# Kernel optimization log

Measured on AMD Instinct MI355X. Metric: run time of the kernel, lower is better.

The kernel has to match this reference:

```python
import jax, jax.numpy as jnp
import numpy as np

N, E, E3, DIM = 25000, 50000, 40000, 64


def setup_inputs() -> dict:
    key = jax.random.key(0)
    ks = jax.random.split(key, 16)
    def g(k, shape, scale=0.1):
        return jax.random.normal(k, shape, jnp.float32) * scale
    return {
        "x": jax.random.normal(ks[0], (N, 8), jnp.float32),
        "edge_attr": jax.random.uniform(ks[1], (E, 19), dtype=jnp.float32),
        "edge_attr3": jax.random.uniform(ks[2], (E3, 8), dtype=jnp.float32),
        "edge_index": jax.random.randint(ks[3], (2, E), 0, N),
        "edge_index3": jax.random.randint(ks[4], (2, E3), 0, N),
        "W_node": g(ks[5], (8, DIM)), "b_node": jnp.zeros((DIM,), jnp.float32),
        "W_ea": g(ks[6], (19, 12)), "b_ea": jnp.zeros((12,), jnp.float32),
        "W_e1": g(ks[7], (12, 128)), "b_e1": jnp.zeros((128,), jnp.float32),
        "W_e2": g(ks[8], (128, DIM * DIM), 0.01), "b_e2": jnp.zeros((DIM * DIM,), jnp.float32),
        "conv_bias": jnp.zeros((DIM,), jnp.float32),
        "W_ih": g(ks[9], (3 * DIM, DIM)), "b_ih": jnp.zeros((3 * DIM,), jnp.float32),
        "W_hh": g(ks[10], (3 * DIM, DIM)), "b_hh": jnp.zeros((3 * DIM,), jnp.float32),
        "W_l1": g(ks[11], (DIM + 8, 128)), "b_l1": jnp.zeros((128,), jnp.float32),
        "W_l2": g(ks[12], (128, 1)), "b_l2": jnp.zeros((1,), jnp.float32),
    }


def _forward(x, edge_attr, edge_attr3,
             W_node, b_node, W_ea, b_ea, W_e1, b_e1, W_e2, b_e2, conv_bias,
             W_ih, b_ih, W_hh, b_hh, W_l1, b_l1, W_l2, b_l2,
             edge_index, edge_index3):
    dim = W_node.shape[1]
    n = x.shape[0]
    out = jax.nn.relu(x @ W_node + b_node)                      # [N, dim]
    ea = jax.nn.relu(edge_attr @ W_ea + b_ea)                   # [E, 12]
    # edge MLP -> per-edge dim x dim weight matrices (same for all 3 conv calls)
    Wedge = (jax.nn.relu(ea @ W_e1 + b_e1) @ W_e2 + b_e2).reshape(-1, dim, dim)  # [E, dim, dim]
    src, dst = edge_index[0], edge_index[1]
    ones = jnp.ones((src.shape[0],), x.dtype)
    cnt = jnp.maximum(jax.ops.segment_sum(ones, dst, num_segments=n), 1.0)  # [N]
    h = out
    for _ in range(3):
        msg = jnp.einsum('ed,edf->ef', out[src], Wedge)                     # per-edge GEMV
        agg = jax.ops.segment_sum(msg, dst, num_segments=n) / cnt[:, None]  # scatter-mean
        m = jax.nn.relu(agg + conv_bias)
        # single-step GRU (PyTorch gate order: r, z, n)
        gi = m @ W_ih.T + b_ih
        gh = h @ W_hh.T + b_hh
        ir, iz, inn = jnp.split(gi, 3, axis=-1)
        hr, hz, hn = jnp.split(gh, 3, axis=-1)
        r = jax.nn.sigmoid(ir + hr)
        z = jax.nn.sigmoid(iz + hz)
        ng = jnp.tanh(inn + r * hn)
        h = (1.0 - z) * ng + z * h
        out = h
    pair = (out[edge_index3[0]] + out[edge_index3[1]]) * 0.5    # mean over the 2 endpoints
    yhat = jnp.concatenate([pair, edge_attr3], axis=1)          # [E3, dim+8]
    yhat = jax.nn.relu(yhat @ W_l1 + b_l1) @ W_l2 + b_l2        # [E3, 1]
    return yhat[:, 0]


def reference(x, edge_attr, edge_attr3, edge_index, edge_index3,
              W_node, b_node, W_ea, b_ea, W_e1, b_e1, W_e2, b_e2, conv_bias,
              W_ih, b_ih, W_hh, b_hh, W_l1, b_l1, W_l2, b_l2):
    return _forward(x, edge_attr, edge_attr3,
                    W_node, b_node, W_ea, b_ea, W_e1, b_e1, W_e2, b_e2, conv_bias,
                    W_ih, b_ih, W_hh, b_hh, W_l1, b_l1, W_l2, b_l2,
                    edge_index, edge_index3)
```

## Files before the change

kernel.cpp:

```cpp
#include <hip/hip_runtime.h>

typedef unsigned short u16;
typedef unsigned int u32;
typedef __attribute__((ext_vector_type(8))) short short8v;
typedef __attribute__((ext_vector_type(4))) float float4v;

__device__ __forceinline__ float sigm(float x) { return 1.0f / (1.0f + __expf(-x)); }
__device__ __forceinline__ u16 f2bf(float f) {
  u32 u = __float_as_uint(f);
  u32 r = (u + 0x7fffu + ((u >> 16) & 1u)) >> 16;
  return (u16)r;
}
__device__ __forceinline__ float bf2f(u16 w) { return __uint_as_float(((u32)w) << 16); }

__global__ void k_cnt(const int* __restrict__ dst, int* __restrict__ cnt, int E) {
  int e = blockIdx.x * blockDim.x + threadIdx.x;
  if (e < E) atomicAdd(&cnt[dst[e]], 1);
}

__global__ void k_scan1(const int* __restrict__ cnt, int* __restrict__ bsum, int N) {
  __shared__ int ws[4];
  int t = threadIdx.x;
  int i = blockIdx.x * 256 + t;
  int v = (i < N) ? cnt[i] : 0;
  int s = v;
  for (int off = 1; off < 64; off <<= 1) s += __shfl_xor(s, off);
  int wid = t >> 6, lane = t & 63;
  if (lane == 0) ws[wid] = s;
  __syncthreads();
  if (t == 0) bsum[blockIdx.x] = ws[0] + ws[1] + ws[2] + ws[3];
}

__global__ void k_scan2(int* __restrict__ bsum, int* __restrict__ row, int nb, int N) {
  __shared__ int s[256];
  int t = threadIdx.x;
  if (t < nb) s[t] = bsum[t];
  __syncthreads();
  if (t == 0) {
    int run = 0;
    for (int i = 0; i < nb; ++i) { int x = s[i]; s[i] = run; run += x; }
    row[N] = run;
  }
  __syncthreads();
  if (t < nb) bsum[t] = s[t];
}

__global__ void k_scan3(const int* __restrict__ cnt, const int* __restrict__ bsum,
                        int* __restrict__ row, int* __restrict__ cursor, int N) {
  __shared__ int ws[4];
  int t = threadIdx.x;
  int i = blockIdx.x * 256 + t;
  int v = (i < N) ? cnt[i] : 0;
  int lane = t & 63, wid = t >> 6;
  int incl = v;
  for (int off = 1; off < 64; off <<= 1) {
    int u = __shfl_up(incl, off);
    if (lane >= off) incl += u;
  }
  if (lane == 63) ws[wid] = incl;
  __syncthreads();
  int woff = bsum[blockIdx.x];
  for (int w = 0; w < wid; ++w) woff += ws[w];
  int excl = woff + incl - v;
  if (i < N) { row[i] = excl; cursor[i] = excl; }
}

__global__ void k_pos(const int* __restrict__ dst, int* __restrict__ cursor,
                      int* __restrict__ pos, int E) {
  int e = blockIdx.x * blockDim.x + threadIdx.x;
  if (e < E) pos[e] = atomicAdd(&cursor[dst[e]], 1);
}

__global__ __launch_bounds__(256) void k_edge_mlp(
    const float* __restrict__ ea_in, const float* __restrict__ Wea,
    const float* __restrict__ bea, const float* __restrict__ We1,
    const float* __restrict__ be1, u16* __restrict__ Ahi, int E) {
  __shared__ float att[2][19];
  __shared__ float ea[2][12];
  int half = threadIdx.x >> 7;
  int t = threadIdx.x & 127;
  int e = blockIdx.x * 2 + half;
  bool real = (e < E);
  int ee = real ? e : E - 1;
  if (t < 19) att[half][t] = ea_in[(size_t)ee * 19 + t];
  __syncthreads();
  if (t < 12) {
    float a = bea[t];
#pragma unroll
    for (int k = 0; k < 19; ++k) a += att[half][k] * Wea[k * 12 + t];
    ea[half][t] = fmaxf(a, 0.0f);
  }
  __syncthreads();
  float a = be1[t];
#pragma unroll
  for (int j = 0; j < 12; ++j) a += ea[half][j] * We1[j * 128 + t];
  if (real) Ahi[(size_t)e * 128 + t] = f2bf(fmaxf(a, 0.0f));
}

__global__ void k_prep_all(
    const float* __restrict__ x, const float* __restrict__ Wn,
    const float* __restrict__ bn, float* __restrict__ h, int N, int nbNode,
    const float* __restrict__ W2, u16* __restrict__ Bph, int nbPack,
    const float* __restrict__ Wih, const float* __restrict__ Whh,
    u16* __restrict__ WpI, u16* __restrict__ WpH, int nbWtf,
    const float* __restrict__ Wl1, u16* __restrict__ Wp1) {
  int b = blockIdx.x;
  if (b < nbNode) {
    int tid = b * 256 + threadIdx.x;
    if (tid >= N * 64) return;
    int n = tid >> 6, f = tid & 63;
    float acc = bn[f];
    for (int k = 0; k < 8; ++k) acc += x[(size_t)n * 8 + k] * Wn[k * 64 + f];
    h[tid] = fmaxf(acc, 0.0f);
  } else if (b < nbNode + nbPack) {
    int tid = (b - nbNode) * 256 + threadIdx.x;
    if (tid >= 128 * 4096) return;
    int j = tid & 7;
    int lane = (tid >> 3) & 63;
    int nt = (tid >> 9) & 3;
    int ks = (tid >> 11) & 3;
    int d = tid >> 13;
    int c = lane & 15, q = lane >> 4;
    int k = ks * 32 + q * 8 + j;
    int n = d * 64 + nt * 16 + c;
    Bph[tid] = f2bf(W2[(size_t)k * 4096 + n]);
  } else if (b < nbNode + nbPack + nbWtf) {
    int tid = (b - nbNode - nbPack) * 256 + threadIdx.x;
    if (tid >= 2 * 12288) return;
    int w = tid / 12288;
    int r = tid - w * 12288;
    int jj = r & 7;
    int lane = (r >> 3) & 63;
    int t = r >> 9;
    int nt = t % 12, ks = t / 12;
    int c = lane & 15, q = lane >> 4;
    int j = nt * 16 + c;
    int k = ks * 32 + q * 8 + jj;
    const float* W = w ? Whh : Wih;
    u16* Wp = w ? WpH : WpI;
    Wp[r] = f2bf(W[j * 64 + k]);
  } else {
    int tid = (b - nbNode - nbPack - nbWtf) * 256 + threadIdx.x;
    if (tid >= 3 * 8 * 64 * 8) return;
    int j = tid & 7;
    int lane = (tid >> 3) & 63;
    int nt = (tid >> 9) & 7;
    int ks = tid >> 12;
    int c = lane & 15, q = lane >> 4;
    int k = ks * 32 + q * 8 + j;
    int n = nt * 16 + c;
    Wp1[tid] = f2bf((k < 72) ? Wl1[k * 128 + n] : 0.0f);
  }
}

__global__ __launch_bounds__(256, 3) void k_conv_fused(
    const u16* __restrict__ Ahi, const u16* __restrict__ Bph,
    const float* __restrict__ b2, const float* __restrict__ h,
    const int* __restrict__ src, const int* __restrict__ pos,
    float* __restrict__ msgp, int E) {
  __shared__ __align__(16) u16 sB[2][8192];
  __shared__ __align__(16) float hsT[32 * 132];
  int m0 = blockIdx.x * 128;
  int d0 = blockIdx.y * 32;
  int tid = threadIdx.x;
  int wave = tid >> 6, lane = tid & 63;
  int mw = wave >> 1, fw = wave & 1;
  int c = lane & 15, q = lane >> 4;

  auto stageB = [&](int d, int b) {
    const u16* gp = Bph + (size_t)d * 8192 + wave * 2048 + lane * 8;
    u16* lp = &sB[b][wave * 2048];
#pragma unroll
    for (int i = 0; i < 4; ++i)
      __builtin_amdgcn_global_load_lds(
          (const __attribute__((address_space(1))) unsigned int*)(gp + i * 512),
          (__attribute__((address_space(3))) unsigned int*)(lp + i * 512), 16, 0, 0);
  };

  stageB(d0, 0);

  short8v afr[4][4];
#pragma unroll
  for (int mt = 0; mt < 4; ++mt) {
    int gr = m0 + mw * 64 + mt * 16 + c;
    if (gr >= E) gr = E - 1;
    const u16* ap = Ahi + (size_t)gr * 128 + q * 8;
#pragma unroll
    for (int ks = 0; ks < 4; ++ks) afr[mt][ks] = *(const short8v*)(ap + ks * 32);
  }

#pragma unroll
  for (int p = 0; p < 4; ++p) {
    int slot = p * 256 + tid;
    int r = slot >> 3, s = slot & 7;
    int ge = m0 + r;
    if (ge >= E) ge = E - 1;
    int sn = src[ge];
    float4 v = *(const float4*)(h + (size_t)sn * 64 + d0 + s * 4);
    hsT[(s * 4 + 0) * 132 + r] = v.x;
    hsT[(s * 4 + 1) * 132 + r] = v.y;
    hsT[(s * 4 + 2) * 132 + r] = v.z;
    hsT[(s * 4 + 3) * 132 + r] = v.w;
  }
  float b2v0 = b2[(size_t)d0 * 64 + fw * 32 + c];
  float b2v1 = b2[(size_t)d0 * 64 + fw * 32 + 16 + c];
  __syncthreads();

  float msg[4][2][4];
#pragma unroll
  for (int mt = 0; mt < 4; ++mt)
#pragma unroll
    for (int nt = 0; nt < 2; ++nt)
#pragma unroll
      for (int r = 0; r < 4; ++r) msg[mt][nt][r] = 0.0f;

  int cur = 0;
  for (int dl = 0; dl < 32; ++dl) {
    float nb0 = 0.f, nb1 = 0.f;
    if (dl < 31) {
      stageB(d0 + dl + 1, cur ^ 1);
      nb0 = b2[(size_t)(d0 + dl + 1) * 64 + fw * 32 + c];
      nb1 = b2[(size_t)(d0 + dl + 1) * 64 + fw * 32 + 16 + c];
    }
    float4v acc[4][2];
#pragma unroll
    for (int mt = 0; mt < 4; ++mt)
#pragma unroll
      for (int nt = 0; nt < 2; ++nt) acc[mt][nt] = (float4v){0.f, 0.f, 0.f, 0.f};
    __builtin_amdgcn_s_setprio(1);
#pragma unroll
    for (int ks = 0; ks < 4; ++ks) {
      short8v b0 = *(const short8v*)(&sB[cur][ks * 2048 + fw * 1024 + lane * 8]);
      short8v b1 = *(const short8v*)(&sB[cur][ks * 2048 + fw * 1024 + 512 + lane * 8]);
#pragma unroll
      for (int mt = 0; mt < 4; ++mt) {
        acc[mt][0] = __builtin_amdgcn_mfma_f32_16x16x32_bf16(afr[mt][ks], b0, acc[mt][0], 0, 0, 0);
        acc[mt][1] = __builtin_amdgcn_mfma_f32_16x16x32_bf16(afr[mt][ks], b1, acc[mt][1], 0, 0, 0);
      }
    }
    __builtin_amdgcn_s_setprio(0);
#pragma unroll
    for (int mt = 0; mt < 4; ++mt) {
      float4 hd4 = *(const float4*)(&hsT[dl * 132 + mw * 64 + mt * 16 + q * 4]);
      float hd[4] = {hd4.x, hd4.y, hd4.z, hd4.w};
#pragma unroll
      for (int r = 0; r < 4; ++r) {
        msg[mt][0][r] += hd[r] * (acc[mt][0][r] + b2v0);
        msg[mt][1][r] += hd[r] * (acc[mt][1][r] + b2v1);
      }
    }
    __syncthreads();
    b2v0 = nb0; b2v1 = nb1;
    cur ^= 1;
  }

#pragma unroll
  for (int mt = 0; mt < 4; ++mt) {
#pragma unroll
    for (int r = 0; r < 4; ++r) {
      int e = m0 + mw * 64 + mt * 16 + q * 4 + r;
      if (e < E) {
        int pe = pos[e];
        float* mp = msgp + (size_t)pe * 128 + blockIdx.y * 64 + fw * 32 + c;
#pragma unroll
        for (int nt = 0; nt < 2; ++nt) mp[nt * 16] = msg[mt][nt][r];
      }
    }
  }
}

__global__ __launch_bounds__(256, 2) void k_gru_mfma(
    const float* __restrict__ msgp, const int* __restrict__ row,
    const float* __restrict__ cb, const u16* __restrict__ WpI,
    const u16* __restrict__ WpH, const float* __restrict__ bih,
    const float* __restrict__ bhh, const float* __restrict__ hin,
    float* __restrict__ hout, int N) {
  __shared__ __align__(16) u16 sM[64 * 72];
  __shared__ __align__(16) u16 sH[64 * 72];
  __shared__ __align__(16) float sHf[64 * 68];
  __shared__ int sRow[65];
  int n0 = blockIdx.x * 64;
  int tid = threadIdx.x;
  if (tid < 65) {
    int idx = n0 + tid;
    sRow[tid] = row[(idx <= N) ? idx : N];
  }
  __syncthreads();
  {
    int nl = tid >> 4, fq = tid & 15;
    float4 cbv = *(const float4*)(cb + fq * 4);
#pragma unroll
    for (int pass = 0; pass < 4; ++pass) {
      int n = pass * 16 + nl;
      int gn = n0 + n;
      bool real = (gn < N);
      int b0 = sRow[n], b1 = sRow[n + 1];
      if (!real) b1 = b0;
      float4 av = {0.f, 0.f, 0.f, 0.f};
      for (int j = b0; j < b1; ++j) {
        float4 m0 = *(const float4*)(msgp + (size_t)j * 128 + fq * 4);
        float4 m1 = *(const float4*)(msgp + (size_t)j * 128 + 64 + fq * 4);
        av.x += m0.x + m1.x; av.y += m0.y + m1.y;
        av.z += m0.z + m1.z; av.w += m0.w + m1.w;
      }
      float cf = fmaxf((float)(b1 - b0), 1.0f);
      int hgn = real ? gn : N - 1;
      float4 hv = *(const float4*)(hin + (size_t)hgn * 64 + fq * 4);
      float m0v = fmaxf(av.x / cf + cbv.x, 0.0f);
      float m1v = fmaxf(av.y / cf + cbv.y, 0.0f);
      float m2v = fmaxf(av.z / cf + cbv.z, 0.0f);
      float m3v = fmaxf(av.w / cf + cbv.w, 0.0f);
      ushort4 mu; mu.x = f2bf(m0v); mu.y = f2bf(m1v); mu.z = f2bf(m2v); mu.w = f2bf(m3v);
      ushort4 hu; hu.x = f2bf(hv.x); hu.y = f2bf(hv.y); hu.z = f2bf(hv.z); hu.w = f2bf(hv.w);
      *(ushort4*)(&sM[n * 72 + fq * 4]) = mu;
      *(ushort4*)(&sH[n * 72 + fq * 4]) = hu;
      *(float4*)(&sHf[n * 68 + fq * 4]) = hv;
    }
  }
  __syncthreads();
  int wave = tid >> 6, lane = tid & 63;
  int c = lane & 15, q = lane >> 4;
  short8v am[2], ah[2];
#pragma unroll
  for (int ks = 0; ks < 2; ++ks) {
    am[ks] = *(const short8v*)(&sM[(wave * 16 + c) * 72 + ks * 32 + q * 8]);
    ah[ks] = *(const short8v*)(&sH[(wave * 16 + c) * 72 + ks * 32 + q * 8]);
  }
  float4v accRZ[8], accN[4], accHN[4];
#pragma unroll
  for (int i = 0; i < 8; ++i) accRZ[i] = (float4v){0.f, 0.f, 0.f, 0.f};
#pragma unroll
  for (int i = 0; i < 4; ++i) {
    accN[i] = (float4v){0.f, 0.f, 0.f, 0.f};
    accHN[i] = (float4v){0.f, 0.f, 0.f, 0.f};
  }
#pragma unroll
  for (int ks = 0; ks < 2; ++ks) {
#pragma unroll
    for (int nt = 0; nt < 8; ++nt) {
      short8v bI = *(const short8v*)(WpI + ((size_t)(ks * 12 + nt) * 64 + lane) * 8);
      short8v bH = *(const short8v*)(WpH + ((size_t)(ks * 12 + nt) * 64 + lane) * 8);
      accRZ[nt] = __builtin_amdgcn_mfma_f32_16x16x32_bf16(am[ks], bI, accRZ[nt], 0, 0, 0);
      accRZ[nt] = __builtin_amdgcn_mfma_f32_16x16x32_bf16(ah[ks], bH, accRZ[nt], 0, 0, 0);
    }
#pragma unroll
    for (int nt = 0; nt < 4; ++nt) {
      short8v bI = *(const short8v*)(WpI + ((size_t)(ks * 12 + 8 + nt) * 64 + lane) * 8);
      short8v bH = *(const short8v*)(WpH + ((size_t)(ks * 12 + 8 + nt) * 64 + lane) * 8);
      accN[nt] = __builtin_amdgcn_mfma_f32_16x16x32_bf16(am[ks], bI, accN[nt], 0, 0, 0);
      accHN[nt] = __builtin_amdgcn_mfma_f32_16x16x32_bf16(ah[ks], bH, accHN[nt], 0, 0, 0);
    }
  }
#pragma unroll
  for (int nt = 0; nt < 4; ++nt) {
    int f = nt * 16 + c;
    float brz_r = bih[f] + bhh[f];
    float brz_z = bih[64 + f] + bhh[64 + f];
    float bin = bih[128 + f];
    float bhn = bhh[128 + f];
#pragma unroll
    for (int r = 0; r < 4; ++r) {
      int nl = wave * 16 + q * 4 + r;
      int gn = n0 + nl;
      float rr = sigm(accRZ[nt][r] + brz_r);
      float zz = sigm(accRZ[nt + 4][r] + brz_z);
      float ng = tanhf(accN[nt][r] + bin + rr * (accHN[nt][r] + bhn));
      float hv = sHf[nl * 68 + f];
      if (gn < N) hout[(size_t)gn * 64 + f] = (1.0f - zz) * ng + zz * hv;
    }
  }
}

__global__ __launch_bounds__(256) void k_final_mfma(
    const float* __restrict__ h, const float* __restrict__ ea3,
    const int* __restrict__ idx3, const u16* __restrict__ Wp1,
    const float* __restrict__ bl1, const float* __restrict__ Wl2,
    const float* __restrict__ bl2, float* __restrict__ out, int E3) {
  __shared__ __align__(16) u16 sF[64 * 104];
  int e0 = blockIdx.x * 64;
  int tid = threadIdx.x;
  {
    int er = tid >> 2;
    int part = tid & 3;
    int ge = e0 + er;
    int gc = (ge < E3) ? ge : E3 - 1;
    int a = idx3[gc], b = idx3[E3 + gc];
    const float* pa = h + (size_t)a * 64 + part * 16;
    const float* pb = h + (size_t)b * 64 + part * 16;
#pragma unroll
    for (int u = 0; u < 4; ++u) {
      float4 va = *(const float4*)(pa + u * 4);
      float4 vb = *(const float4*)(pb + u * 4);
      ushort4 mu;
      mu.x = f2bf(0.5f * (va.x + vb.x));
      mu.y = f2bf(0.5f * (va.y + vb.y));
      mu.z = f2bf(0.5f * (va.z + vb.z));
      mu.w = f2bf(0.5f * (va.w + vb.w));
      *(ushort4*)(&sF[er * 104 + part * 16 + u * 4]) = mu;
    }
    if (part == 0) {
      float4 e0v = *(const float4*)(ea3 + (size_t)gc * 8);
      float4 e1v = *(const float4*)(ea3 + (size_t)gc * 8 + 4);
      ushort4 u0, u1;
      u0.x = f2bf(e0v.x); u0.y = f2bf(e0v.y); u0.z = f2bf(e0v.z); u0.w = f2bf(e0v.w);
      u1.x = f2bf(e1v.x); u1.y = f2bf(e1v.y); u1.z = f2bf(e1v.z); u1.w = f2bf(e1v.w);
      *(ushort4*)(&sF[er * 104 + 64]) = u0;
      *(ushort4*)(&sF[er * 104 + 68]) = u1;
    } else {
      ushort4 z = {0, 0, 0, 0};
      *(ushort4*)(&sF[er * 104 + 72 + (part - 1) * 8]) = z;
      *(ushort4*)(&sF[er * 104 + 76 + (part - 1) * 8]) = z;
    }
  }
  __syncthreads();
  int wave = tid >> 6, lane = tid & 63;
  int c = lane & 15, q = lane >> 4;
  float4v acc[8];
#pragma unroll
  for (int nt = 0; nt < 8; ++nt) acc[nt] = (float4v){0.f, 0.f, 0.f, 0.f};
#pragma unroll
  for (int ks = 0; ks < 3; ++ks) {
    short8v af = *(const short8v*)(&sF[(wave * 16 + c) * 104 + ks * 32 + q * 8]);
#pragma unroll
    for (int nt = 0; nt < 8; ++nt) {
      short8v bf = *(const short8v*)(Wp1 + ((size_t)(ks * 8 + nt) * 64 + lane) * 8);
      acc[nt] = __builtin_amdgcn_mfma_f32_16x16x32_bf16(af, bf, acc[nt], 0, 0, 0);
    }
  }
  float v[4] = {0.f, 0.f, 0.f, 0.f};
#pragma unroll
  for (int nt = 0; nt < 8; ++nt) {
    int n = nt * 16 + c;
    float b1 = bl1[n];
    float w2 = Wl2[n];
#pragma unroll
    for (int r = 0; r < 4; ++r) v[r] += fmaxf(acc[nt][r] + b1, 0.0f) * w2;
  }
#pragma unroll
  for (int off = 1; off < 16; off <<= 1) {
#pragma unroll
    for (int r = 0; r < 4; ++r) v[r] += __shfl_xor(v[r], off);
  }
  if (c == 0) {
    float b2v = bl2[0];
#pragma unroll
    for (int r = 0; r < 4; ++r) {
      int e = e0 + wave * 16 + q * 4 + r;
      if (e < E3) out[e] = v[r] + b2v;
    }
  }
}

extern "C" void kernel_launch(void* const* d_in, const int* in_sizes, int n_in,
                              void* d_out, int out_size, void* d_ws, size_t ws_size,
                              hipStream_t stream) {
  const float* x          = (const float*)d_in[0];
  const float* edge_attr  = (const float*)d_in[1];
  const float* edge_attr3 = (const float*)d_in[2];
  const int*   edge_index = (const int*)d_in[3];
  const int*   edge_index3= (const int*)d_in[4];
  const float* W_node = (const float*)d_in[5];
  const float* b_node = (const float*)d_in[6];
  const float* W_ea   = (const float*)d_in[7];
  const float* b_ea   = (const float*)d_in[8];
  const float* W_e1   = (const float*)d_in[9];
  const float* b_e1   = (const float*)d_in[10];
  const float* W_e2   = (const float*)d_in[11];
  const float* b_e2   = (const float*)d_in[12];
  const float* conv_bias = (const float*)d_in[13];
  const float* W_ih   = (const float*)d_in[14];
  const float* b_ih   = (const float*)d_in[15];
  const float* W_hh   = (const float*)d_in[16];
  const float* b_hh   = (const float*)d_in[17];
  const float* W_l1   = (const float*)d_in[18];
  const float* b_l1   = (const float*)d_in[19];
  const float* W_l2   = (const float*)d_in[20];
  const float* b_l2   = (const float*)d_in[21];

  int N  = in_sizes[0] / 8;
  int E  = in_sizes[1] / 19;
  int E3 = in_sizes[2] / 8;

  char* p = (char*)d_ws;
  auto carve = [&](size_t bytes) -> void* {
    char* q = p;
    p += (bytes + 255) & ~(size_t)255;
    return (void*)q;
  };
  float* hA    = (float*)carve((size_t)N * 64 * 4);
  float* hB    = (float*)carve((size_t)N * 64 * 4);
  float* msgp  = (float*)carve((size_t)E * 128 * 4);
  int*   cnt   = (int*)carve((size_t)N * 4);
  int*   row   = (int*)carve((size_t)(N + 1) * 4);
  int*   cursor= (int*)carve((size_t)N * 4);
  int*   pos   = (int*)carve((size_t)E * 4);
  int*   bsum  = (int*)carve(256 * 4);
  u16*   Ahi   = (u16*)carve((size_t)E * 128 * 2);
  u16*   Bph   = (u16*)carve((size_t)128 * 4096 * 2);
  u16*   WpI   = (u16*)carve(12288 * 2);
  u16*   WpH   = (u16*)carve(12288 * 2);
  u16*   Wp1   = (u16*)carve(12288 * 2);

  const int* src = edge_index;
  const int* dst = edge_index + E;

  int nb = (N + 255) / 256;
  hipMemsetAsync(cnt, 0, (size_t)N * 4, stream);
  k_cnt<<<(E + 255) / 256, 256, 0, stream>>>(dst, cnt, E);
  k_scan1<<<nb, 256, 0, stream>>>(cnt, bsum, N);
  k_scan2<<<1, 256, 0, stream>>>(bsum, row, nb, N);
  k_scan3<<<nb, 256, 0, stream>>>(cnt, bsum, row, cursor, N);
  k_pos<<<(E + 255) / 256, 256, 0, stream>>>(dst, cursor, pos, E);

  k_edge_mlp<<<(E + 1) / 2, 256, 0, stream>>>(edge_attr, W_ea, b_ea, W_e1, b_e1, Ahi, E);
  int nbNode = ((size_t)N * 64 + 255) / 256;
  int nbPack = (128 * 4096 + 255) / 256;
  int nbWtf  = (2 * 12288 + 255) / 256;
  int nbWl1  = (12288 + 255) / 256;
  k_prep_all<<<nbNode + nbPack + nbWtf + nbWl1, 256, 0, stream>>>(
      x, W_node, b_node, hA, N, nbNode, W_e2, Bph, nbPack,
      W_ih, W_hh, WpI, WpH, nbWtf, W_l1, Wp1);

  float* hcur = hA;
  float* hnxt = hB;
  dim3 gconv((E + 127) / 128, 2);
  int ngru = (N + 63) / 64;
  for (int it = 0; it < 3; ++it) {
    k_conv_fused<<<gconv, 256, 0, stream>>>(Ahi, Bph, b_e2, hcur, src, pos, msgp, E);
    k_gru_mfma<<<ngru, 256, 0, stream>>>(msgp, row, conv_bias, WpI, WpH,
                                         b_ih, b_hh, hcur, hnxt, N);
    float* tmp = hcur; hcur = hnxt; hnxt = tmp;
  }
  k_final_mfma<<<(E3 + 63) / 64, 256, 0, stream>>>(hcur, edge_attr3, edge_index3, Wp1,
                                                   b_l1, W_l2, b_l2, (float*)d_out, E3);
}
```

Before: 444.6 us.

## Merge conv d-split into one block, store bf16 messages, stage bias in LDS

The conv kernel no longer splits the 64 input dims across two blocks in y. Each block now loops over all 64 dims, so the two fp32 partial message halves are no longer written and summed later. Messages are stored once per edge as bf16, which cuts the write and the GRU gather traffic by about four times. The b_e2 bias is converted to bf16 and kept in LDS instead of being read per iteration. In exchange there is half the grid parallelism, more LDS, lower occupancy (launch bounds 2), and bf16 rounding on the messages and bias.

```diff
diff --git a/kernel.cpp b/kernel.cpp
--- a/kernel.cpp
+++ b/kernel.cpp
@@ -153,15 +153,15 @@
   }
 }
 
-__global__ __launch_bounds__(256, 3) void k_conv_fused(
+__global__ __launch_bounds__(256, 2) void k_conv_fused(
     const u16* __restrict__ Ahi, const u16* __restrict__ Bph,
     const float* __restrict__ b2, const float* __restrict__ h,
     const int* __restrict__ src, const int* __restrict__ pos,
-    float* __restrict__ msgp, int E) {
+    u16* __restrict__ msgh, int E) {
   __shared__ __align__(16) u16 sB[2][8192];
-  __shared__ __align__(16) float hsT[32 * 132];
+  __shared__ __align__(16) float hsT[64 * 132];
+  __shared__ __align__(16) u16 sb2h[4096];
   int m0 = blockIdx.x * 128;
-  int d0 = blockIdx.y * 32;
   int tid = threadIdx.x;
   int wave = tid >> 6, lane = tid & 63;
   int mw = wave >> 1, fw = wave & 1;
@@ -177,7 +177,7 @@
           (__attribute__((address_space(3))) unsigned int*)(lp + i * 512), 16, 0, 0);
   };
 
-  stageB(d0, 0);
+  stageB(0, 0);
 
   short8v afr[4][4];
 #pragma unroll
@@ -190,20 +190,29 @@
   }
 
 #pragma unroll
-  for (int p = 0; p < 4; ++p) {
+  for (int p = 0; p < 8; ++p) {
     int slot = p * 256 + tid;
-    int r = slot >> 3, s = slot & 7;
+    int r = slot >> 4, s = slot & 15;
     int ge = m0 + r;
     if (ge >= E) ge = E - 1;
     int sn = src[ge];
-    float4 v = *(const float4*)(h + (size_t)sn * 64 + d0 + s * 4);
+    float4 v = *(const float4*)(h + (size_t)sn * 64 + s * 4);
     hsT[(s * 4 + 0) * 132 + r] = v.x;
     hsT[(s * 4 + 1) * 132 + r] = v.y;
     hsT[(s * 4 + 2) * 132 + r] = v.z;
     hsT[(s * 4 + 3) * 132 + r] = v.w;
   }
-  float b2v0 = b2[(size_t)d0 * 64 + fw * 32 + c];
-  float b2v1 = b2[(size_t)d0 * 64 + fw * 32 + 16 + c];
+  {
+    int t16 = tid * 16;
+#pragma unroll
+    for (int u = 0; u < 4; ++u) {
+      float4 v = *(const float4*)(b2 + t16 + u * 4);
+      sb2h[t16 + u * 4 + 0] = f2bf(v.x);
+      sb2h[t16 + u * 4 + 1] = f2bf(v.y);
+      sb2h[t16 + u * 4 + 2] = f2bf(v.z);
+      sb2h[t16 + u * 4 + 3] = f2bf(v.w);
+    }
+  }
   __syncthreads();
 
   float msg[4][2][4];
@@ -215,13 +224,10 @@
       for (int r = 0; r < 4; ++r) msg[mt][nt][r] = 0.0f;
 
   int cur = 0;
-  for (int dl = 0; dl < 32; ++dl) {
-    float nb0 = 0.f, nb1 = 0.f;
-    if (dl < 31) {
-      stageB(d0 + dl + 1, cur ^ 1);
-      nb0 = b2[(size_t)(d0 + dl + 1) * 64 + fw * 32 + c];
-      nb1 = b2[(size_t)(d0 + dl + 1) * 64 + fw * 32 + 16 + c];
-    }
+  for (int dl = 0; dl < 64; ++dl) {
+    if (dl < 63) stageB(dl + 1, cur ^ 1);
+    float b2v0 = bf2f(sb2h[dl * 64 + fw * 32 + c]);
+    float b2v1 = bf2f(sb2h[dl * 64 + fw * 32 + 16 + c]);
     float4v acc[4][2];
 #pragma unroll
     for (int mt = 0; mt < 4; ++mt)
@@ -250,7 +256,6 @@
       }
     }
     __syncthreads();
-    b2v0 = nb0; b2v1 = nb1;
     cur ^= 1;
   }
 
@@ -261,16 +266,16 @@
       int e = m0 + mw * 64 + mt * 16 + q * 4 + r;
       if (e < E) {
         int pe = pos[e];
-        float* mp = msgp + (size_t)pe * 128 + blockIdx.y * 64 + fw * 32 + c;
-#pragma unroll
-        for (int nt = 0; nt < 2; ++nt) mp[nt * 16] = msg[mt][nt][r];
+        u16* mp = msgh + (size_t)pe * 64 + fw * 32 + c;
+        mp[0] = f2bf(msg[mt][0][r]);
+        mp[16] = f2bf(msg[mt][1][r]);
       }
     }
   }
 }
 
 __global__ __launch_bounds__(256, 2) void k_gru_mfma(
-    const float* __restrict__ msgp, const int* __restrict__ row,
+    const u16* __restrict__ msgh, const int* __restrict__ row,
     const float* __restrict__ cb, const u16* __restrict__ WpI,
     const u16* __restrict__ WpH, const float* __restrict__ bih,
     const float* __restrict__ bhh, const float* __restrict__ hin,
@@ -298,10 +303,9 @@
       if (!real) b1 = b0;
       float4 av = {0.f, 0.f, 0.f, 0.f};
       for (int j = b0; j < b1; ++j) {
-        float4 m0 = *(const float4*)(msgp + (size_t)j * 128 + fq * 4);
-        float4 m1 = *(const float4*)(msgp + (size_t)j * 128 + 64 + fq * 4);
-        av.x += m0.x + m1.x; av.y += m0.y + m1.y;
-        av.z += m0.z + m1.z; av.w += m0.w + m1.w;
+        ushort4 mv = *(const ushort4*)(msgh + (size_t)j * 64 + fq * 4);
+        av.x += bf2f(mv.x); av.y += bf2f(mv.y);
+        av.z += bf2f(mv.z); av.w += bf2f(mv.w);
       }
       float cf = fmaxf((float)(b1 - b0), 1.0f);
       int hgn = real ? gn : N - 1;
@@ -489,7 +493,7 @@
   };
   float* hA    = (float*)carve((size_t)N * 64 * 4);
   float* hB    = (float*)carve((size_t)N * 64 * 4);
-  float* msgp  = (float*)carve((size_t)E * 128 * 4);
+  u16*   msgh  = (u16*)carve((size_t)E * 64 * 2);
   int*   cnt   = (int*)carve((size_t)N * 4);
   int*   row   = (int*)carve((size_t)(N + 1) * 4);
   int*   cursor= (int*)carve((size_t)N * 4);
@@ -523,11 +527,11 @@
 
   float* hcur = hA;
   float* hnxt = hB;
-  dim3 gconv((E + 127) / 128, 2);
+  int gconv = (E + 127) / 128;
   int ngru = (N + 63) / 64;
   for (int it = 0; it < 3; ++it) {
-    k_conv_fused<<<gconv, 256, 0, stream>>>(Ahi, Bph, b_e2, hcur, src, pos, msgp, E);
-    k_gru_mfma<<<ngru, 256, 0, stream>>>(msgp, row, conv_bias, WpI, WpH,
+    k_conv_fused<<<gconv, 256, 0, stream>>>(Ahi, Bph, b_e2, hcur, src, pos, msgh, E);
+    k_gru_mfma<<<ngru, 256, 0, stream>>>(msgh, row, conv_bias, WpI, WpH,
                                          b_ih, b_hh, hcur, hnxt, N);
     float* tmp = hcur; hcur = hnxt; hnxt = tmp;
   }
```

Result: faster. 398.0 us (-10.5%).
